# Performance work log

Measured on AMD Instinct MI355X. Metric: run time of the kernel, lower is better.

Reference implementation:

```python
import jax, jax.numpy as jnp
import numpy as np

THRESHOLD = 1e-3  # hardcoded `thresholds = 0.001` in the sparse branch


def setup_inputs() -> dict:
    key = jax.random.key(0)
    k1, k2, k3, k4, k5 = jax.random.split(key, 5)
    b, r, d_in, d_out = 8, 4096, 768, 768
    x = jax.random.normal(k1, (b, r, d_in), dtype=jnp.float32)
    weight = jax.random.normal(k2, (d_out, d_in), dtype=jnp.float32) * 0.02
    bias = jax.random.normal(k3, (d_out,), dtype=jnp.float32) * 0.02
    U = jax.random.normal(k4, (d_in, d_in), dtype=jnp.float32) * (d_in ** -0.5)
    VT = jax.random.normal(k5, (d_out, d_out), dtype=jnp.float32) * (d_out ** -0.5)
    return {"x": x, "weight": weight, "bias": bias, "U": U, "VT": VT}


def reference(x, weight, bias, U, VT):
    # Sparse path (len_grads >= 30) of LinearFunctionSparseGrad.forward.
    # h = x @ U.T, rotated into the gradient basis.  [b, r, c]
    h = jnp.einsum('brc,dc->brd', x, U)
    # Threshold-sparsify: zero entries with |h| <= 0.001.
    h = jnp.where(jnp.abs(h) > THRESHOLD, h, jnp.zeros((), h.dtype))
    # Original: gather nonzero rows/cols, h[rows][:, cols] @ weight.T[cols],
    # then scatter back via I[:, rows] @ res_. Dropped cols are exactly-zero
    # columns and dropped rows are exactly-zero rows, so the math equals a
    # dense matmul on the masked tensor (no [b*r, b*r] identity needed).
    res = jnp.einsum('brc,oc->bro', h, weight)        # h @ weight.T
    res = jnp.einsum('bro,po->brp', res, VT)          # res_ @ VT.T (self.VT=VT_orig.T => VT here)
    return res + bias
```

## Files before the change

### kernel.cpp

```cpp
#include <hip/hip_runtime.h>
#include <hip/hip_bf16.h>

typedef __bf16 bf16_t;
typedef bf16_t bf16x8 __attribute__((ext_vector_type(8)));
typedef bf16_t bf16x4 __attribute__((ext_vector_type(4)));
typedef float  f32x4  __attribute__((ext_vector_type(4)));

#define BM 128
#define BN 128
#define BK 64

enum { EPI_NONE = 0, EPI_THRESH = 1, EPI_BIAS = 2 };


template <int EPI, typename CT>
__device__ __forceinline__
void gemm_tile(const bf16_t* __restrict__ A, const bf16_t* __restrict__ B,
               CT* __restrict__ C, const float* __restrict__ bias,
               int m0, int n0, int N, int K,
               bf16_t* As, bf16_t* Bs)
{
    const int lane = threadIdx.x & 63;
    const int wave = threadIdx.x >> 6;
    const int wm = wave >> 1;
    const int wn = wave & 1;

    const int srow = lane >> 3;
    const int scg  = (lane & 7) ^ ((lane >> 3) & 7);

    const int fm = lane & 15;
    const int q  = lane >> 4;
    const int fsw = fm & 7;

    f32x4 acc[4][4];
#pragma unroll
    for (int i = 0; i < 4; i++)
#pragma unroll
        for (int j = 0; j < 4; j++) acc[i][j] = {0.f, 0.f, 0.f, 0.f};

    for (int k0 = 0; k0 < K; k0 += BK) {
#pragma unroll
        for (int i = 0; i < 4; i++) {
            const int ubase = wave * 256 + i * 64;
            const int row   = (ubase >> 3) + srow;
            const bf16_t* ga = A + (size_t)(m0 + row) * K + k0 + scg * 8;
            __builtin_amdgcn_global_load_lds(
                (const __attribute__((address_space(1))) void*)ga,
                (__attribute__((address_space(3))) void*)(As + (size_t)ubase * 8),
                16, 0, 0);
            const bf16_t* gb = B + (size_t)(n0 + row) * K + k0 + scg * 8;
            __builtin_amdgcn_global_load_lds(
                (const __attribute__((address_space(1))) void*)gb,
                (__attribute__((address_space(3))) void*)(Bs + (size_t)ubase * 8),
                16, 0, 0);
        }
        __syncthreads();

#pragma unroll
        for (int h = 0; h < 2; h++) {
            bf16x8 af[4], bfr[4];
#pragma unroll
            for (int i = 0; i < 4; i++) {
                const int row = wm * 64 + i * 16 + fm;
                af[i] = *(const bf16x8*)(As + (size_t)(row * 8 + ((h * 4 + q) ^ fsw)) * 8);
            }
#pragma unroll
            for (int j = 0; j < 4; j++) {
                const int row = wn * 64 + j * 16 + fm;
                bfr[j] = *(const bf16x8*)(Bs + (size_t)(row * 8 + ((h * 4 + q) ^ fsw)) * 8);
            }
#pragma unroll
            for (int i = 0; i < 4; i++)
#pragma unroll
                for (int j = 0; j < 4; j++)
                    acc[i][j] = __builtin_amdgcn_mfma_f32_16x16x32_bf16(
                        af[i], bfr[j], acc[i][j], 0, 0, 0);
        }
        __syncthreads();
    }

#pragma unroll
    for (int i = 0; i < 4; i++) {
#pragma unroll
        for (int j = 0; j < 4; j++) {
            const int col = n0 + wn * 64 + j * 16 + fm;
            float bv = 0.f;
            if (EPI == EPI_BIAS) bv = bias[col];
#pragma unroll
            for (int r = 0; r < 4; r++) {
                const int row = m0 + wm * 64 + i * 16 + q * 4 + r;
                float v = acc[i][j][r];
                if (EPI == EPI_THRESH) v = (fabsf(v) > 1e-3f) ? v : 0.f;
                if (EPI == EPI_BIAS) v += bv;
                C[(size_t)row * N + col] = (CT)v;
            }
        }
    }
}

__global__ __launch_bounds__(256)
void gemm_h_wc(const bf16_t* __restrict__ xb, const bf16_t* __restrict__ Ub,
               bf16_t* __restrict__ h,
               const bf16_t* __restrict__ VTb, const bf16_t* __restrict__ Wt,
               bf16_t* __restrict__ Wc)
{
    __shared__ __align__(16) bf16_t As[BM * BK];
    __shared__ __align__(16) bf16_t Bs[BN * BK];
    const int b = blockIdx.x;
    if (b < 1536) {
        gemm_tile<EPI_THRESH, bf16_t>(xb, Ub, h, nullptr,
                                      (b / 6) * BM, (b % 6) * BN, 768, 768, As, Bs);
    } else {
        const int b2 = b - 1536;
        gemm_tile<EPI_NONE, bf16_t>(VTb, Wt, Wc, nullptr,
                                    (b2 / 6) * BM, (b2 % 6) * BN, 768, 768, As, Bs);
    }
}

__global__ __launch_bounds__(256)
void gemm_out(const bf16_t* __restrict__ h, const bf16_t* __restrict__ Wc,
              float* __restrict__ out, const float* __restrict__ bias)
{
    __shared__ __align__(16) bf16_t As[BM * BK];
    __shared__ __align__(16) bf16_t Bs[BN * BK];
    const int b = blockIdx.x;
    gemm_tile<EPI_BIAS, float>(h, Wc, out, bias,
                               (b / 6) * BM, (b % 6) * BN, 768, 768, As, Bs);
}

__global__ __launch_bounds__(256)
void prep(const float* __restrict__ x, const float* __restrict__ U,
          const float* __restrict__ VT, const float* __restrict__ w,
          bf16_t* __restrict__ xb, bf16_t* __restrict__ Ub,
          bf16_t* __restrict__ VTb, bf16_t* __restrict__ Wt)
{
    __shared__ float tt[32][33];
    const int b = blockIdx.x;
    if (b < 25728) {
        const float* src; bf16_t* dst; int i;
        if (b < 24576)      { src = x;  dst = xb;  i = b * 256 + threadIdx.x; }
        else if (b < 25152) { src = U;  dst = Ub;  i = (b - 24576) * 256 + threadIdx.x; }
        else                { src = VT; dst = VTb; i = (b - 25152) * 256 + threadIdx.x; }
        const f32x4 v = ((const f32x4*)src)[i];
        bf16x4 o;
        o[0] = (bf16_t)v[0]; o[1] = (bf16_t)v[1];
        o[2] = (bf16_t)v[2]; o[3] = (bf16_t)v[3];
        ((bf16x4*)dst)[i] = o;
    } else {
        const int t = b - 25728;
        const int bx = (t % 24) * 32, by = (t / 24) * 32;
        const int tx = threadIdx.x & 31, ty = threadIdx.x >> 5;
#pragma unroll
        for (int i = 0; i < 32; i += 8)
            tt[ty + i][tx] = w[(size_t)(by + ty + i) * 768 + bx + tx];
        __syncthreads();
#pragma unroll
        for (int i = 0; i < 32; i += 8)
            Wt[(size_t)(bx + ty + i) * 768 + by + tx] = (bf16_t)tt[tx][ty + i];
    }
}

extern "C" void kernel_launch(void* const* d_in, const int* in_sizes, int n_in,
                              void* d_out, int out_size, void* d_ws, size_t ws_size,
                              hipStream_t stream)
{
    const float* x    = (const float*)d_in[0];
    const float* w    = (const float*)d_in[1];
    const float* bias = (const float*)d_in[2];
    const float* U    = (const float*)d_in[3];
    const float* VT   = (const float*)d_in[4];
    float* out = (float*)d_out;

    const int D = 768;
    const int M = 8 * 4096;
    const size_t MD = (size_t)M * D;
    const size_t DD = (size_t)D * D;

    char* ws = (char*)d_ws;
    bf16_t* xb  = (bf16_t*)ws;
    bf16_t* h   = (bf16_t*)(ws + MD * 2);
    bf16_t* Ub  = (bf16_t*)(ws + MD * 4);
    bf16_t* VTb = (bf16_t*)(ws + MD * 4 + DD * 2);
    bf16_t* Wt  = (bf16_t*)(ws + MD * 4 + DD * 4);
    bf16_t* Wc  = (bf16_t*)(ws + MD * 4 + DD * 6);

    prep<<<26304, 256, 0, stream>>>(x, U, VT, w, xb, Ub, VTb, Wt);
    gemm_h_wc<<<1536 + 36, 256, 0, stream>>>(xb, Ub, h, VTb, Wt, Wc);
    gemm_out<<<1536, 256, 0, stream>>>(h, Wc, out, bias);
}
```

Baseline: 309.3 us.

## Use 256x128 tiles with triple-buffered LDS prefetch pipeline and XCD-aware block remap

Doubles the GEMM M-tile to 256 rows with 512-thread blocks and adds a three-stage LDS ring buffer. Direct global-to-LDS loads for k-step t+2 are issued in two halves interleaved with the MFMA phases, with explicit vmcnt waits, raw barriers and s_setprio around the MFMA bursts. Block indices are remapped so neighbouring tiles land on the same XCD, aiming for better L2 reuse of shared operand rows. The goal is to hide global load latency and cut per-tile load overhead. In exchange, LDS use grows to about 147 KB per block, which limits occupancy to one block per CU.

```diff
diff --git a/kernel.cpp b/kernel.cpp
--- a/kernel.cpp
+++ b/kernel.cpp
@@ -6,88 +6,163 @@
 typedef bf16_t bf16x4 __attribute__((ext_vector_type(4)));
 typedef float  f32x4  __attribute__((ext_vector_type(4)));
 
-#define BM 128
+#define BM 256
 #define BN 128
 #define BK 64
 
 enum { EPI_NONE = 0, EPI_THRESH = 1, EPI_BIAS = 2 };
 
+__device__ __forceinline__ void memfence() { asm volatile("" ::: "memory"); }
+__device__ __forceinline__ void blockbar() {
+    memfence(); __builtin_amdgcn_s_barrier(); memfence();
+}
+
+#define GLD16(src, dst) __builtin_amdgcn_global_load_lds( \
+    (const __attribute__((address_space(1))) void*)(src), \
+    (__attribute__((address_space(3))) void*)(dst), 16, 0, 0)
 
 template <int EPI, typename CT>
 __device__ __forceinline__
 void gemm_tile(const bf16_t* __restrict__ A, const bf16_t* __restrict__ B,
                CT* __restrict__ C, const float* __restrict__ bias,
                int m0, int n0, int N, int K,
-               bf16_t* As, bf16_t* Bs)
+               bf16_t* __restrict__ As, bf16_t* __restrict__ Bs)
 {
     const int lane = threadIdx.x & 63;
     const int wave = threadIdx.x >> 6;
     const int wm = wave >> 1;
     const int wn = wave & 1;
 
-    const int srow = lane >> 3;
-    const int scg  = (lane & 7) ^ ((lane >> 3) & 7);
-
-    const int fm = lane & 15;
-    const int q  = lane >> 4;
+    const int fm  = lane & 15;
+    const int q   = lane >> 4;
     const int fsw = fm & 7;
 
+    const int NT = K / BK;
+
+    const bf16_t* gsrc[6];
+    int ldst[6];
+#pragma unroll
+    for (int s = 0; s < 6; ++s) {
+        const int g = wave + 8 * s;
+        if (s < 4) {
+            const int u = g * 64 + lane;
+            const int row = u >> 3;
+            const int ch  = (u & 7) ^ (row & 7);
+            gsrc[s] = A + (size_t)(m0 + row) * K + ch * 8;
+            ldst[s] = g * 512;
+        } else {
+            const int u = (g - 32) * 64 + lane;
+            const int row = u >> 3;
+            const int ch  = (u & 7) ^ (row & 7);
+            gsrc[s] = B + (size_t)(n0 + row) * K + ch * 8;
+            ldst[s] = (g - 32) * 512;
+        }
+    }
+
     f32x4 acc[4][4];
 #pragma unroll
-    for (int i = 0; i < 4; i++)
-#pragma unroll
-        for (int j = 0; j < 4; j++) acc[i][j] = {0.f, 0.f, 0.f, 0.f};
-
-    for (int k0 = 0; k0 < K; k0 += BK) {
-#pragma unroll
-        for (int i = 0; i < 4; i++) {
-            const int ubase = wave * 256 + i * 64;
-            const int row   = (ubase >> 3) + srow;
-            const bf16_t* ga = A + (size_t)(m0 + row) * K + k0 + scg * 8;
-            __builtin_amdgcn_global_load_lds(
-                (const __attribute__((address_space(1))) void*)ga,
-                (__attribute__((address_space(3))) void*)(As + (size_t)ubase * 8),
-                16, 0, 0);
-            const bf16_t* gb = B + (size_t)(n0 + row) * K + k0 + scg * 8;
-            __builtin_amdgcn_global_load_lds(
-                (const __attribute__((address_space(1))) void*)gb,
-                (__attribute__((address_space(3))) void*)(Bs + (size_t)ubase * 8),
-                16, 0, 0);
-        }
-        __syncthreads();
-
-#pragma unroll
-        for (int h = 0; h < 2; h++) {
-            bf16x8 af[4], bfr[4];
-#pragma unroll
-            for (int i = 0; i < 4; i++) {
-                const int row = wm * 64 + i * 16 + fm;
-                af[i] = *(const bf16x8*)(As + (size_t)(row * 8 + ((h * 4 + q) ^ fsw)) * 8);
-            }
-#pragma unroll
-            for (int j = 0; j < 4; j++) {
-                const int row = wn * 64 + j * 16 + fm;
-                bfr[j] = *(const bf16x8*)(Bs + (size_t)(row * 8 + ((h * 4 + q) ^ fsw)) * 8);
-            }
-#pragma unroll
-            for (int i = 0; i < 4; i++)
-#pragma unroll
-                for (int j = 0; j < 4; j++)
+    for (int i = 0; i < 4; ++i)
+#pragma unroll
+        for (int j = 0; j < 4; ++j) acc[i][j] = (f32x4){0.f, 0.f, 0.f, 0.f};
+
+#pragma unroll
+    for (int s = 0; s < 6; ++s) {
+        GLD16(gsrc[s], (s < 4 ? As : Bs) + ldst[s]);
+        gsrc[s] += BK;
+    }
+#pragma unroll
+    for (int s = 0; s < 6; ++s) {
+        GLD16(gsrc[s], (s < 4 ? As + 256 * 64 : Bs + 128 * 64) + ldst[s]);
+        gsrc[s] += BK;
+    }
+    asm volatile("s_waitcnt vmcnt(6)" ::: "memory");
+    blockbar();
+
+    int bc = 0;
+    for (int t = 0; t < NT; ++t) {
+        const bf16_t* __restrict__ Ab = As + bc * (256 * 64);
+        const bf16_t* __restrict__ Bb = Bs + bc * (128 * 64);
+        const int bs2 = (bc >= 1) ? bc - 1 : 2;
+        bf16_t* Asd = As + bs2 * (256 * 64);
+        bf16_t* Bsd = Bs + bs2 * (128 * 64);
+        const bool do_stage = (t + 2 < NT);
+
+        bf16x8 af[4][2], bfr[2][2];
+
+#pragma unroll
+        for (int i = 0; i < 4; ++i) {
+            const int row = wm * 64 + i * 16 + fm;
+#pragma unroll
+            for (int kk = 0; kk < 2; ++kk)
+                af[i][kk] = *(const bf16x8*)(Ab + (size_t)(row * 8 + ((kk * 4 + q) ^ fsw)) * 8);
+        }
+#pragma unroll
+        for (int j = 0; j < 2; ++j) {
+            const int row = wn * 64 + j * 16 + fm;
+#pragma unroll
+            for (int kk = 0; kk < 2; ++kk)
+                bfr[j][kk] = *(const bf16x8*)(Bb + (size_t)(row * 8 + ((kk * 4 + q) ^ fsw)) * 8);
+        }
+        if (do_stage) {
+            GLD16(gsrc[0], Asd + ldst[0]); gsrc[0] += BK;
+            GLD16(gsrc[1], Asd + ldst[1]); gsrc[1] += BK;
+            GLD16(gsrc[4], Bsd + ldst[4]); gsrc[4] += BK;
+        }
+        blockbar();
+        __builtin_amdgcn_s_setprio(1);
+#pragma unroll
+        for (int i = 0; i < 4; ++i)
+#pragma unroll
+            for (int j = 0; j < 2; ++j)
+#pragma unroll
+                for (int kk = 0; kk < 2; ++kk)
                     acc[i][j] = __builtin_amdgcn_mfma_f32_16x16x32_bf16(
-                        af[i], bfr[j], acc[i][j], 0, 0, 0);
-        }
-        __syncthreads();
-    }
-
-#pragma unroll
-    for (int i = 0; i < 4; i++) {
-#pragma unroll
-        for (int j = 0; j < 4; j++) {
+                        af[i][kk], bfr[j][kk], acc[i][j], 0, 0, 0);
+        __builtin_amdgcn_s_setprio(0);
+        blockbar();
+
+#pragma unroll
+        for (int j = 0; j < 2; ++j) {
+            const int row = wn * 64 + (j + 2) * 16 + fm;
+#pragma unroll
+            for (int kk = 0; kk < 2; ++kk)
+                bfr[j][kk] = *(const bf16x8*)(Bb + (size_t)(row * 8 + ((kk * 4 + q) ^ fsw)) * 8);
+        }
+        if (do_stage) {
+            GLD16(gsrc[2], Asd + ldst[2]); gsrc[2] += BK;
+            GLD16(gsrc[3], Asd + ldst[3]); gsrc[3] += BK;
+            GLD16(gsrc[5], Bsd + ldst[5]); gsrc[5] += BK;
+        }
+        blockbar();
+        __builtin_amdgcn_s_setprio(1);
+#pragma unroll
+        for (int i = 0; i < 4; ++i)
+#pragma unroll
+            for (int j = 0; j < 2; ++j)
+#pragma unroll
+                for (int kk = 0; kk < 2; ++kk)
+                    acc[i][j + 2] = __builtin_amdgcn_mfma_f32_16x16x32_bf16(
+                        af[i][kk], bfr[j][kk], acc[i][j + 2], 0, 0, 0);
+        __builtin_amdgcn_s_setprio(0);
+
+        if (t < NT - 1) {
+            asm volatile("s_waitcnt lgkmcnt(0)" ::: "memory");
+            if (do_stage) asm volatile("s_waitcnt vmcnt(6)" ::: "memory");
+            else          asm volatile("s_waitcnt vmcnt(0)" ::: "memory");
+            blockbar();
+        }
+        bc = (bc >= 2) ? 0 : bc + 1;
+    }
+
+#pragma unroll
+    for (int i = 0; i < 4; ++i) {
+#pragma unroll
+        for (int j = 0; j < 4; ++j) {
             const int col = n0 + wn * 64 + j * 16 + fm;
             float bv = 0.f;
             if (EPI == EPI_BIAS) bv = bias[col];
 #pragma unroll
-            for (int r = 0; r < 4; r++) {
+            for (int r = 0; r < 4; ++r) {
                 const int row = m0 + wm * 64 + i * 16 + q * 4 + r;
                 float v = acc[i][j][r];
                 if (EPI == EPI_THRESH) v = (fabsf(v) > 1e-3f) ? v : 0.f;
@@ -98,34 +173,36 @@
     }
 }
 
-__global__ __launch_bounds__(256)
+__global__ __launch_bounds__(512, 2)
 void gemm_h_wc(const bf16_t* __restrict__ xb, const bf16_t* __restrict__ Ub,
                bf16_t* __restrict__ h,
                const bf16_t* __restrict__ VTb, const bf16_t* __restrict__ Wt,
                bf16_t* __restrict__ Wc)
 {
-    __shared__ __align__(16) bf16_t As[BM * BK];
-    __shared__ __align__(16) bf16_t Bs[BN * BK];
+    __shared__ __align__(16) bf16_t As[3 * 256 * 64];
+    __shared__ __align__(16) bf16_t Bs[3 * 128 * 64];
     const int b = blockIdx.x;
-    if (b < 1536) {
+    if (b < 768) {
+        const int L = (b & 7) * 96 + (b >> 3);
         gemm_tile<EPI_THRESH, bf16_t>(xb, Ub, h, nullptr,
-                                      (b / 6) * BM, (b % 6) * BN, 768, 768, As, Bs);
+                                      (L / 6) * BM, (L % 6) * BN, 768, 768, As, Bs);
     } else {
-        const int b2 = b - 1536;
+        const int b2 = b - 768;
         gemm_tile<EPI_NONE, bf16_t>(VTb, Wt, Wc, nullptr,
                                     (b2 / 6) * BM, (b2 % 6) * BN, 768, 768, As, Bs);
     }
 }
 
-__global__ __launch_bounds__(256)
+__global__ __launch_bounds__(512, 2)
 void gemm_out(const bf16_t* __restrict__ h, const bf16_t* __restrict__ Wc,
               float* __restrict__ out, const float* __restrict__ bias)
 {
-    __shared__ __align__(16) bf16_t As[BM * BK];
-    __shared__ __align__(16) bf16_t Bs[BN * BK];
+    __shared__ __align__(16) bf16_t As[3 * 256 * 64];
+    __shared__ __align__(16) bf16_t Bs[3 * 128 * 64];
     const int b = blockIdx.x;
+    const int L = (b & 7) * 96 + (b >> 3);
     gemm_tile<EPI_BIAS, float>(h, Wc, out, bias,
-                               (b / 6) * BM, (b % 6) * BN, 768, 768, As, Bs);
+                               (L / 6) * BM, (L % 6) * BN, 768, 768, As, Bs);
 }
 
 __global__ __launch_bounds__(256)
@@ -185,6 +262,6 @@
     bf16_t* Wc  = (bf16_t*)(ws + MD * 4 + DD * 6);
 
     prep<<<26304, 256, 0, stream>>>(x, U, VT, w, xb, Ub, VTb, Wt);
-    gemm_h_wc<<<1536 + 36, 256, 0, stream>>>(xb, Ub, h, VTb, Wt, Wc);
-    gemm_out<<<1536, 256, 0, stream>>>(h, Wc, out, bias);
-}
+    gemm_h_wc<<<768 + 18, 512, 0, stream>>>(xb, Ub, h, VTb, Wt, Wc);
+    gemm_out<<<768, 512, 0, stream>>>(h, Wc, out, bias);
+}
```

Result: faster. 294.2 us (-4.9%).

## Use double-buffered 256x256 GEMM tiles with phased MFMA schedule and XCD remap

Applied to the files above, without the earlier changes.

Enlarges GEMM tiles from 128x128 to 256x256 with 512-thread blocks, so each staged tile of A and B is reused across more MFMAs. LDS is double-buffered so the next K tile is prefetched with async global-to-LDS loads while the current one is computed. Each K step is split into four phases that interleave LDS fragment loads, barriers and setprio-raised MFMA bursts. Block indices are remapped across XCDs to improve L2 locality. The cost is 128KB of LDS per block, which allows only one block per CU, and 384 blocks over the CUs leave an uneven last wave.

```diff
diff --git a/kernel.cpp b/kernel.cpp
--- a/kernel.cpp
+++ b/kernel.cpp
@@ -6,126 +6,180 @@
 typedef bf16_t bf16x4 __attribute__((ext_vector_type(4)));
 typedef float  f32x4  __attribute__((ext_vector_type(4)));
 
-#define BM 128
-#define BN 128
+#define BM 256
+#define BN 256
 #define BK 64
 
 enum { EPI_NONE = 0, EPI_THRESH = 1, EPI_BIAS = 2 };
 
+__device__ __forceinline__ void memfence() { asm volatile("" ::: "memory"); }
+__device__ __forceinline__ void blockbar() {
+    memfence(); __builtin_amdgcn_s_barrier(); memfence();
+}
+
+#define GLD16(src, dst) __builtin_amdgcn_global_load_lds( \
+    (const __attribute__((address_space(1))) void*)(src), \
+    (__attribute__((address_space(3))) void*)(dst), 16, 0, 0)
 
 template <int EPI, typename CT>
 __device__ __forceinline__
 void gemm_tile(const bf16_t* __restrict__ A, const bf16_t* __restrict__ B,
                CT* __restrict__ C, const float* __restrict__ bias,
                int m0, int n0, int N, int K,
-               bf16_t* As, bf16_t* Bs)
+               bf16_t* __restrict__ As, bf16_t* __restrict__ Bs)
 {
     const int lane = threadIdx.x & 63;
     const int wave = threadIdx.x >> 6;
-    const int wm = wave >> 1;
-    const int wn = wave & 1;
-
-    const int srow = lane >> 3;
-    const int scg  = (lane & 7) ^ ((lane >> 3) & 7);
-
-    const int fm = lane & 15;
-    const int q  = lane >> 4;
+    const int wm = wave >> 2;
+    const int wn = wave & 3;
+
+    const int fm  = lane & 15;
+    const int ql  = lane >> 4;
     const int fsw = fm & 7;
 
-    f32x4 acc[4][4];
-#pragma unroll
-    for (int i = 0; i < 4; i++)
-#pragma unroll
-        for (int j = 0; j < 4; j++) acc[i][j] = {0.f, 0.f, 0.f, 0.f};
-
-    for (int k0 = 0; k0 < K; k0 += BK) {
-#pragma unroll
-        for (int i = 0; i < 4; i++) {
-            const int ubase = wave * 256 + i * 64;
-            const int row   = (ubase >> 3) + srow;
-            const bf16_t* ga = A + (size_t)(m0 + row) * K + k0 + scg * 8;
-            __builtin_amdgcn_global_load_lds(
-                (const __attribute__((address_space(1))) void*)ga,
-                (__attribute__((address_space(3))) void*)(As + (size_t)ubase * 8),
-                16, 0, 0);
-            const bf16_t* gb = B + (size_t)(n0 + row) * K + k0 + scg * 8;
-            __builtin_amdgcn_global_load_lds(
-                (const __attribute__((address_space(1))) void*)gb,
-                (__attribute__((address_space(3))) void*)(Bs + (size_t)ubase * 8),
-                16, 0, 0);
-        }
-        __syncthreads();
-
-#pragma unroll
-        for (int h = 0; h < 2; h++) {
-            bf16x8 af[4], bfr[4];
-#pragma unroll
-            for (int i = 0; i < 4; i++) {
-                const int row = wm * 64 + i * 16 + fm;
-                af[i] = *(const bf16x8*)(As + (size_t)(row * 8 + ((h * 4 + q) ^ fsw)) * 8);
-            }
-#pragma unroll
-            for (int j = 0; j < 4; j++) {
-                const int row = wn * 64 + j * 16 + fm;
-                bfr[j] = *(const bf16x8*)(Bs + (size_t)(row * 8 + ((h * 4 + q) ^ fsw)) * 8);
-            }
-#pragma unroll
-            for (int i = 0; i < 4; i++)
-#pragma unroll
-                for (int j = 0; j < 4; j++)
-                    acc[i][j] = __builtin_amdgcn_mfma_f32_16x16x32_bf16(
-                        af[i], bfr[j], acc[i][j], 0, 0, 0);
-        }
-        __syncthreads();
-    }
-
-#pragma unroll
-    for (int i = 0; i < 4; i++) {
-#pragma unroll
-        for (int j = 0; j < 4; j++) {
-            const int col = n0 + wn * 64 + j * 16 + fm;
+    const int NT = K / BK;
+
+    const int choff = ((lane & 7) ^ ((lane >> 3) & 7)) * 8;
+    const bf16_t* pA[2]; const bf16_t* pB[2];
+    int sd[2];
+#pragma unroll
+    for (int l = 0; l < 2; ++l) {
+        const int r = (wave * 2 + l) * 8 + (lane >> 3);
+        pA[l] = A + (size_t)(m0 + r) * K + choff;
+        pB[l] = B + (size_t)(n0 + r) * K + choff;
+        sd[l] = (wave * 2 + l) * 64;
+    }
+
+#define STAGE_TILE(tt, Ad, Bd) do {                                          \
+    _Pragma("unroll") for (int h_ = 0; h_ < 2; ++h_)                         \
+    _Pragma("unroll") for (int l_ = 0; l_ < 2; ++l_) {                       \
+        GLD16(pA[l_] + (size_t)h_ * 128 * K + (size_t)(tt) * BK,             \
+              (Ad) + (size_t)(h_ * 1024 + sd[l_]) * 8);                      \
+        GLD16(pB[l_] + (size_t)h_ * 128 * K + (size_t)(tt) * BK,             \
+              (Bd) + (size_t)(h_ * 1024 + sd[l_]) * 8);                      \
+    } } while (0)
+
+#define LOAD_A(mh) do {                                                      \
+    _Pragma("unroll") for (int i_ = 0; i_ < 4; ++i_)                         \
+    _Pragma("unroll") for (int k_ = 0; k_ < 2; ++k_)                         \
+        af[i_][k_] = *(const bf16x8*)(Ab + (size_t)(                         \
+            (wm * 128 + (mh) * 64 + i_ * 16 + fm) * 8 +                      \
+            ((k_ * 4 + ql) ^ fsw)) * 8); } while (0)
+
+#define LOAD_B(nh) do {                                                      \
+    _Pragma("unroll") for (int j_ = 0; j_ < 2; ++j_)                         \
+    _Pragma("unroll") for (int k_ = 0; k_ < 2; ++k_)                         \
+        bfx[j_][k_] = *(const bf16x8*)(Bb + (size_t)(                        \
+            (wn * 64 + (nh) * 32 + j_ * 16 + fm) * 8 +                       \
+            ((k_ * 4 + ql) ^ fsw)) * 8); } while (0)
+
+#define MFMA_Q(mh, nh) do {                                                  \
+    _Pragma("unroll") for (int i_ = 0; i_ < 4; ++i_)                         \
+    _Pragma("unroll") for (int j_ = 0; j_ < 2; ++j_)                         \
+    _Pragma("unroll") for (int k_ = 0; k_ < 2; ++k_)                         \
+        acc[(mh) * 4 + i_][(nh) * 2 + j_] =                                  \
+            __builtin_amdgcn_mfma_f32_16x16x32_bf16(                         \
+                af[i_][k_], bfx[j_][k_],                                     \
+                acc[(mh) * 4 + i_][(nh) * 2 + j_], 0, 0, 0); } while (0)
+
+#define PHASE_TAIL(mh, nh) do {                                              \
+    blockbar();                                                              \
+    asm volatile("s_waitcnt lgkmcnt(0)" ::: "memory");                       \
+    __builtin_amdgcn_sched_barrier(0);                                       \
+    __builtin_amdgcn_s_setprio(1);                                           \
+    MFMA_Q(mh, nh);                                                          \
+    __builtin_amdgcn_s_setprio(0);                                           \
+    blockbar(); } while (0)
+
+    f32x4 acc[8][4];
+#pragma unroll
+    for (int i = 0; i < 8; ++i)
+#pragma unroll
+        for (int j = 0; j < 4; ++j) acc[i][j] = (f32x4){0.f, 0.f, 0.f, 0.f};
+
+    STAGE_TILE(0, As, Bs);
+    asm volatile("s_waitcnt vmcnt(0)" ::: "memory");
+    blockbar();
+
+    for (int t = 0; t < NT; ++t) {
+        const int cur = t & 1;
+        const bf16_t* __restrict__ Ab = As + cur * (BM * BK);
+        const bf16_t* __restrict__ Bb = Bs + cur * (BN * BK);
+        bf16_t* Asd = As + (cur ^ 1) * (BM * BK);
+        bf16_t* Bsd = Bs + (cur ^ 1) * (BN * BK);
+
+        bf16x8 af[4][2], bfx[2][2];
+
+        LOAD_A(0); LOAD_B(0);
+        if (t + 1 < NT) STAGE_TILE(t + 1, Asd, Bsd);
+        PHASE_TAIL(0, 0);
+
+        LOAD_B(1);
+        PHASE_TAIL(0, 1);
+
+        LOAD_A(1);
+        PHASE_TAIL(1, 1);
+
+        LOAD_B(0);
+        asm volatile("s_waitcnt vmcnt(0)" ::: "memory");
+        PHASE_TAIL(1, 0);
+    }
+
+#pragma unroll
+    for (int mi = 0; mi < 8; ++mi) {
+#pragma unroll
+        for (int ni = 0; ni < 4; ++ni) {
+            const int col = n0 + wn * 64 + ni * 16 + fm;
             float bv = 0.f;
             if (EPI == EPI_BIAS) bv = bias[col];
 #pragma unroll
-            for (int r = 0; r < 4; r++) {
-                const int row = m0 + wm * 64 + i * 16 + q * 4 + r;
-                float v = acc[i][j][r];
+            for (int r = 0; r < 4; ++r) {
+                const int row = m0 + wm * 128 + mi * 16 + ql * 4 + r;
+                float v = acc[mi][ni][r];
                 if (EPI == EPI_THRESH) v = (fabsf(v) > 1e-3f) ? v : 0.f;
                 if (EPI == EPI_BIAS) v += bv;
                 C[(size_t)row * N + col] = (CT)v;
             }
         }
     }
-}
-
-__global__ __launch_bounds__(256)
+
+#undef STAGE_TILE
+#undef LOAD_A
+#undef LOAD_B
+#undef MFMA_Q
+#undef PHASE_TAIL
+}
+
+__global__ __launch_bounds__(512, 2)
 void gemm_h_wc(const bf16_t* __restrict__ xb, const bf16_t* __restrict__ Ub,
                bf16_t* __restrict__ h,
                const bf16_t* __restrict__ VTb, const bf16_t* __restrict__ Wt,
                bf16_t* __restrict__ Wc)
 {
-    __shared__ __align__(16) bf16_t As[BM * BK];
-    __shared__ __align__(16) bf16_t Bs[BN * BK];
+    __shared__ __align__(16) bf16_t As[2 * BM * BK];
+    __shared__ __align__(16) bf16_t Bs[2 * BN * BK];
     const int b = blockIdx.x;
-    if (b < 1536) {
+    if (b < 384) {
+        const int L = (b & 7) * 48 + (b >> 3);
         gemm_tile<EPI_THRESH, bf16_t>(xb, Ub, h, nullptr,
-                                      (b / 6) * BM, (b % 6) * BN, 768, 768, As, Bs);
+                                      (L / 3) * BM, (L % 3) * BN, 768, 768, As, Bs);
     } else {
-        const int b2 = b - 1536;
+        const int b2 = b - 384;
         gemm_tile<EPI_NONE, bf16_t>(VTb, Wt, Wc, nullptr,
-                                    (b2 / 6) * BM, (b2 % 6) * BN, 768, 768, As, Bs);
-    }
-}
-
-__global__ __launch_bounds__(256)
+                                    (b2 / 3) * BM, (b2 % 3) * BN, 768, 768, As, Bs);
+    }
+}
+
+__global__ __launch_bounds__(512, 2)
 void gemm_out(const bf16_t* __restrict__ h, const bf16_t* __restrict__ Wc,
               float* __restrict__ out, const float* __restrict__ bias)
 {
-    __shared__ __align__(16) bf16_t As[BM * BK];
-    __shared__ __align__(16) bf16_t Bs[BN * BK];
+    __shared__ __align__(16) bf16_t As[2 * BM * BK];
+    __shared__ __align__(16) bf16_t Bs[2 * BN * BK];
     const int b = blockIdx.x;
+    const int L = (b & 7) * 48 + (b >> 3);
     gemm_tile<EPI_BIAS, float>(h, Wc, out, bias,
-                               (b / 6) * BM, (b % 6) * BN, 768, 768, As, Bs);
+                               (L / 3) * BM, (L % 3) * BN, 768, 768, As, Bs);
 }
 
 __global__ __launch_bounds__(256)
@@ -185,6 +239,6 @@
     bf16_t* Wc  = (bf16_t*)(ws + MD * 4 + DD * 6);
 
     prep<<<26304, 256, 0, stream>>>(x, U, VT, w, xb, Ub, VTb, Wt);
-    gemm_h_wc<<<1536 + 36, 256, 0, stream>>>(xb, Ub, h, VTb, Wt, Wc);
-    gemm_out<<<1536, 256, 0, stream>>>(h, Wc, out, bias);
-}
+    gemm_h_wc<<<384 + 9, 512, 0, stream>>>(xb, Ub, h, VTb, Wt, Wc);
+    gemm_out<<<384, 512, 0, stream>>>(h, Wc, out, bias);
+}
```

New measurement: 299.8 us. -3.1%, faster.
